# Kernel optimization log

Measured on AMD Instinct MI355X. Metric: run time of the kernel, lower is better.

Reference implementation:

```python
import jax, jax.numpy as jnp
import numpy as np

SYNCNET_T = 5
EMB_D = 512


def _l2norm(x, eps=1e-12):
    return x / jnp.maximum(jnp.linalg.norm(x, axis=-1, keepdims=True), eps)


def setup_inputs() -> dict:
    key = jax.random.key(0)
    k = jax.random.split(key, 6)
    b = 256
    a_1 = jax.random.normal(k[0], (b, 1, 80, 16), dtype=jnp.float32)
    a_2 = jax.random.normal(k[1], (b, 1, 80, 16), dtype=jnp.float32)
    v_1 = jax.random.normal(k[2], (b, 3, SYNCNET_T, 96, 96), dtype=jnp.float32)
    v_2 = jax.random.normal(k[3], (b, 3, SYNCNET_T, 96, 96), dtype=jnp.float32)
    da = 1 * 80 * 16
    dv = 3 * SYNCNET_T * 48 * 96
    W_a = jax.random.normal(k[4], (da, EMB_D), dtype=jnp.float32) / np.float32(np.sqrt(da))
    W_v = jax.random.normal(k[5], (dv, EMB_D), dtype=jnp.float32) / np.float32(np.sqrt(dv))
    return {"a_1": a_1, "v_1": v_1, "a_2": a_2, "v_2": v_2, "W_a": W_a, "W_v": W_v}


def reference(a_1, v_1, a_2, v_2, W_a, W_v):
    b = a_1.shape[0]
    audio = jnp.concatenate([a_1, a_2], axis=0)      # (2b,1,80,16)
    visual = jnp.concatenate([v_1, v_2], axis=0)     # (2b,3,T,96,96)
    visual = visual[:, :, :, visual.shape[3] // 2:]  # lower half -> (2b,3,T,48,96)
    # torch.cat([visual[:,:,i] for i in range(T)], dim=1) -> channel order (T,3)
    n2 = visual.shape[0]
    visual = jnp.moveaxis(visual, 2, 1).reshape(n2, 3 * SYNCNET_T, 48, 96)
    # syncnet (modeled): flatten -> linear -> L2 normalize, 512-d embeddings
    a = _l2norm(audio.reshape(n2, -1) @ W_a)  # (2b,d)
    v = _l2norm(visual.reshape(n2, -1) @ W_v)  # (2b,d)
    a1, a2 = a[:b], a[b:]
    v1, v2 = v[:b], v[b:]
    dot = lambda x, y: jnp.sum(x * y, axis=-1)
    # numerator: product of {a1,a2}x{v1,v2} + combos within audio and within visual
    numerator = (jnp.exp(dot(a1, v1)) + jnp.exp(dot(a1, v2))
                 + jnp.exp(dot(a2, v1)) + jnp.exp(dot(a2, v2))
                 + jnp.exp(dot(a1, a2)) + jnp.exp(dot(v1, v2)))  # (b,)
    # denominator: product of {a1,a2} with ALL visual embeddings v (2b)
    denominator = (jnp.exp(a1 @ v.T) + jnp.exp(a2 @ v.T)).sum(axis=1)  # (b,)
    loss = -jnp.mean(jnp.log(numerator / denominator))
    return loss
```

## Files before the change

### kernel.cpp

```cpp
#include <hip/hip_runtime.h>

typedef __attribute__((ext_vector_type(8))) short bf16x8;
typedef __attribute__((ext_vector_type(4))) float f32x4;

#define KSPLIT_V 16
#define KSPLIT_A 4

__device__ __forceinline__ unsigned int pk2(float a, float b) {
    unsigned int r;
    asm("v_cvt_pk_bf16_f32 %0, %1, %2" : "=v"(r) : "v"(a), "v"(b));
    return r;
}

template<int MODE>
__global__ __launch_bounds__(256, 4) void mm_kernel(
    const float* __restrict__ s1, const float* __restrict__ s2,
    const float* __restrict__ Bsrc, float* __restrict__ outp,
    float* __restrict__ den, float* __restrict__ num)
{
    __shared__ uint4 As[2][256];
    __shared__ uint4 Bs[2][256];

    const int tid = threadIdx.x;
    const int blk = blockIdx.x;

    int m0, n0, k0, nsteps, z = 0;
    if (MODE == 0) {
        const int lin = (blk & 7) * 128 + (blk >> 3);
        z  = lin >> 6;
        m0 = ((lin >> 3) & 7) * 64;
        n0 = (lin & 7) * 64;
        k0 = z * 4320;
        nsteps = 135;
    } else if (MODE == 1) {
        z  = blk >> 6;
        m0 = ((blk >> 3) & 7) * 64;
        n0 = (blk & 7) * 64;
        k0 = z * 320;
        nsteps = 10;
    } else {
        m0 = (blk >> 3) * 64;
        n0 = (blk & 7) * 64;
        k0 = 0;
        nsteps = 16;
    }
    if (MODE != 2) outp += (size_t)z * (512 * 512);

    const int ROWSTR = (MODE == 0) ? 138240 : (MODE == 1 ? 1280 : 512);

    const int a_row = tid >> 2;
    const int a_kb  = tid & 3;
    const int b_col = tid & 63;
    const int b_kb  = tid >> 6;
    const int a_u = (a_kb * 64 + a_row) ^ (a_kb << 1);
    const int b_u = (b_kb * 64 + b_col) ^ (b_kb << 1);

    const int grow = m0 + a_row;
    const float* abase = (grow < 256) ? (s1 + (size_t)grow * ROWSTR)
                                      : (s2 + (size_t)(grow - 256) * ROWSTR);
    int aoff, jj = 0, kglob = k0;
    if (MODE == 0) {
        const int ph = k0 / 4608;
        jj = k0 - ph * 4608;
        const int c = ph % 3, t = ph / 3;
        aoff = c * 46080 + t * 9216 + 4608 + jj + a_kb * 8;
    } else {
        aoff = k0 + a_kb * 8;
    }

    const float* bptr;
    if (MODE == 2) bptr = Bsrc + (size_t)(n0 + b_col) * 512 + b_kb * 8;
    else           bptr = Bsrc + (size_t)(k0 + b_kb * 8) * 512 + n0 + b_col;

    const int lane = tid & 63;
    const int wid  = tid >> 6;
    const int wrow = (wid >> 1) * 32;
    const int wcol = (wid & 1) * 32;
    const int l15  = lane & 15;
    const int lk   = lane >> 4;

    int ra[2], rb[2];
    #pragma unroll
    for (int m = 0; m < 2; ++m) ra[m] = (lk * 64 + wrow + m * 16 + l15) ^ (lk << 1);
    #pragma unroll
    for (int n = 0; n < 2; ++n) rb[n] = (lk * 64 + wcol + n * 16 + l15) ^ (lk << 1);

    f32x4 acc[2][2];
    #pragma unroll
    for (int m = 0; m < 2; ++m)
        #pragma unroll
        for (int n = 0; n < 2; ++n) acc[m][n] = f32x4{0.f, 0.f, 0.f, 0.f};

    float4 A0 = *(const float4*)(abase + aoff);
    float4 A1 = *(const float4*)(abase + aoff + 4);
    float4 B0, B1; float bsr[8];
    if (MODE == 2) {
        B0 = *(const float4*)bptr; B1 = *(const float4*)(bptr + 4);
    } else {
        #pragma unroll
        for (int j = 0; j < 8; ++j) bsr[j] = bptr[(size_t)j * 512];
    }

    for (int ks = 0; ks < nsteps; ++ks) {
        const int cur = ks & 1;

        const bool more = (ks + 1 < nsteps);
        float4 A0n, A1n, B0n, B1n; float bsn[8];
        if (more) {
            kglob += 32;
            if (MODE == 0) {
                aoff += 32; jj += 32;
                if (jj == 4608) {
                    jj = 0;
                    const int ph = kglob / 4608;
                    const int c = ph % 3, t = ph / 3;
                    aoff = c * 46080 + t * 9216 + 4608 + a_kb * 8;
                }
            } else {
                aoff += 32;
            }
            A0n = *(const float4*)(abase + aoff);
            A1n = *(const float4*)(abase + aoff + 4);
            if (MODE == 2) {
                bptr += 32;
                B0n = *(const float4*)bptr; B1n = *(const float4*)(bptr + 4);
            } else {
                bptr += 32 * 512;
                #pragma unroll
                for (int j = 0; j < 8; ++j) bsn[j] = bptr[(size_t)j * 512];
            }
        }

        uint4 pa;
        pa.x = pk2(A0.x, A0.y); pa.y = pk2(A0.z, A0.w);
        pa.z = pk2(A1.x, A1.y); pa.w = pk2(A1.z, A1.w);
        As[cur][a_u] = pa;
        uint4 pb;
        if (MODE == 2) {
            pb.x = pk2(B0.x, B0.y); pb.y = pk2(B0.z, B0.w);
            pb.z = pk2(B1.x, B1.y); pb.w = pk2(B1.z, B1.w);
        } else {
            pb.x = pk2(bsr[0], bsr[1]); pb.y = pk2(bsr[2], bsr[3]);
            pb.z = pk2(bsr[4], bsr[5]); pb.w = pk2(bsr[6], bsr[7]);
        }
        Bs[cur][b_u] = pb;
        __syncthreads();

        bf16x8 af[2], bfr[2];
        #pragma unroll
        for (int m = 0; m < 2; ++m) af[m] = __builtin_bit_cast(bf16x8, As[cur][ra[m]]);
        #pragma unroll
        for (int n = 0; n < 2; ++n) bfr[n] = __builtin_bit_cast(bf16x8, Bs[cur][rb[n]]);
        #pragma unroll
        for (int m = 0; m < 2; ++m)
            #pragma unroll
            for (int n = 0; n < 2; ++n)
                acc[m][n] = __builtin_amdgcn_mfma_f32_16x16x32_bf16(af[m], bfr[n], acc[m][n], 0, 0, 0);

        if (more) {
            A0 = A0n; A1 = A1n;
            if (MODE == 2) { B0 = B0n; B1 = B1n; }
            else {
                #pragma unroll
                for (int j = 0; j < 8; ++j) bsr[j] = bsn[j];
            }
        }
    }

    if (MODE != 2) {
        #pragma unroll
        for (int m = 0; m < 2; ++m)
            #pragma unroll
            for (int n = 0; n < 2; ++n) {
                const int col = n0 + wcol + n * 16 + l15;
                #pragma unroll
                for (int r = 0; r < 4; ++r) {
                    const int row = m0 + wrow + m * 16 + lk * 4 + r;
                    outp[(size_t)row * 512 + col] = acc[m][n][r];
                }
            }
    } else {
        #pragma unroll
        for (int m = 0; m < 2; ++m) {
            float rs[4] = {0.f, 0.f, 0.f, 0.f};
            #pragma unroll
            for (int n = 0; n < 2; ++n) {
                const int col = n0 + wcol + n * 16 + l15;
                #pragma unroll
                for (int r = 0; r < 4; ++r) {
                    const int row = m0 + wrow + m * 16 + lk * 4 + r;
                    const float e = __expf(acc[m][n][r]);
                    rs[r] += e;
                    if (((row - col) & 255) == 0) atomicAdd(num + (row & 255), e);
                }
            }
            #pragma unroll
            for (int r = 0; r < 4; ++r) {
                float v = rs[r];
                v += __shfl_xor(v, 1);
                v += __shfl_xor(v, 2);
                v += __shfl_xor(v, 4);
                v += __shfl_xor(v, 8);
                if (l15 == 0) {
                    const int row = m0 + wrow + m * 16 + lk * 4 + r;
                    atomicAdd(den + (row & 255), v);
                }
            }
        }
    }
}

__global__ __launch_bounds__(256) void norm_kernel(
    const float* __restrict__ partA, const float* __restrict__ partV,
    float* __restrict__ Aout, float* __restrict__ Vout)
{
    const int row = blockIdx.x;
    const int tid = threadIdx.x;
    const bool isV = row >= 512;
    const int r = isV ? (row - 512) : row;
    const int c0 = tid, c1 = tid + 256;

    float v0 = 0.f, v1 = 0.f;
    if (isV) {
        #pragma unroll
        for (int zz = 0; zz < KSPLIT_V; ++zz) {
            const float* p = partV + (size_t)zz * 262144 + (size_t)r * 512;
            v0 += p[c0]; v1 += p[c1];
        }
    } else {
        #pragma unroll
        for (int zz = 0; zz < KSPLIT_A; ++zz) {
            const float* p = partA + (size_t)zz * 262144 + (size_t)r * 512;
            v0 += p[c0]; v1 += p[c1];
        }
    }

    float ss = v0 * v0 + v1 * v1;
    #pragma unroll
    for (int off = 32; off > 0; off >>= 1) ss += __shfl_down(ss, off);
    __shared__ float sbuf[4];
    if ((tid & 63) == 0) sbuf[tid >> 6] = ss;
    __syncthreads();
    const float total = sbuf[0] + sbuf[1] + sbuf[2] + sbuf[3];
    const float inv = 1.f / fmaxf(sqrtf(total), 1e-12f);

    float* outp = (isV ? Vout : Aout) + (size_t)r * 512;
    outp[c0] = v0 * inv;
    outp[c1] = v1 * inv;
}

__global__ __launch_bounds__(512) void zero_kernel(float* __restrict__ p) {
    p[threadIdx.x] = 0.f;
}

__global__ __launch_bounds__(256) void dots_kernel(
    const float* __restrict__ A, const float* __restrict__ V,
    float* __restrict__ num)
{
    const int b = blockIdx.x;
    const int i = b & 255;
    const float* X = (b < 256) ? A : V;
    const float* x = X + (size_t)i * 512;
    const float* y = X + (size_t)(i + 256) * 512;
    const int tid = threadIdx.x;
    float d = x[tid] * y[tid] + x[tid + 256] * y[tid + 256];
    #pragma unroll
    for (int off = 32; off > 0; off >>= 1) d += __shfl_down(d, off);
    __shared__ float sbuf[4];
    if ((tid & 63) == 0) sbuf[tid >> 6] = d;
    __syncthreads();
    if (tid == 0) atomicAdd(num + i, __expf(sbuf[0] + sbuf[1] + sbuf[2] + sbuf[3]));
}

__global__ __launch_bounds__(256) void final_kernel(
    const float* __restrict__ den, const float* __restrict__ num,
    float* __restrict__ out)
{
    const int tid = threadIdx.x;
    float v = logf(den[tid]) - logf(num[tid]);
    #pragma unroll
    for (int off = 32; off > 0; off >>= 1) v += __shfl_down(v, off);
    __shared__ float sbuf[4];
    if ((tid & 63) == 0) sbuf[tid >> 6] = v;
    __syncthreads();
    if (tid == 0) out[0] = (sbuf[0] + sbuf[1] + sbuf[2] + sbuf[3]) * (1.f / 256.f);
}

extern "C" void kernel_launch(void* const* d_in, const int* in_sizes, int n_in,
                              void* d_out, int out_size, void* d_ws, size_t ws_size,
                              hipStream_t stream)
{
    (void)in_sizes; (void)n_in; (void)out_size; (void)ws_size;
    const float* a_1 = (const float*)d_in[0];
    const float* v_1 = (const float*)d_in[1];
    const float* a_2 = (const float*)d_in[2];
    const float* v_2 = (const float*)d_in[3];
    const float* W_a = (const float*)d_in[4];
    const float* W_v = (const float*)d_in[5];
    float* out = (float*)d_out;

    float* ws      = (float*)d_ws;
    float* partV   = ws;
    float* partA   = partV + (size_t)KSPLIT_V * 262144;
    float* Anorm   = partA + (size_t)KSPLIT_A * 262144;
    float* Vnorm   = Anorm + 262144;
    float* den     = Vnorm + 262144;
    float* num     = den + 256;

    zero_kernel<<<1, 512, 0, stream>>>(den);
    mm_kernel<0><<<1024, 256, 0, stream>>>(v_1, v_2, W_v, partV, nullptr, nullptr);
    mm_kernel<1><<<256, 256, 0, stream>>>(a_1, a_2, W_a, partA, nullptr, nullptr);
    norm_kernel<<<1024, 256, 0, stream>>>(partA, partV, Anorm, Vnorm);
    mm_kernel<2><<<64, 256, 0, stream>>>(Anorm, Anorm + 256 * 512, Vnorm, nullptr, den, num);
    dots_kernel<<<512, 256, 0, stream>>>(Anorm, Vnorm, num);
    final_kernel<<<1, 256, 0, stream>>>(den, num, out);
}
```

Baseline: 176.0 us.

## Pipeline GEMM global loads with inline asm and raise visual K-split

Rewrites the main loop of the split-K GEMM as a two-stage ping-pong over two shared-memory buffers. Global loads are issued through inline-asm `dwordx4`/`dword` instructions with immediate offsets, and explicit `vmcnt` waits let the next tile's loads overlap the pack, sync and MFMA of the current tile. The visual GEMM's K-split goes from 16 to 24 with 90 steps each, and launch bounds rise to 6 waves per SIMD, both to add parallelism and occupancy. The cost is extra partial-sum traffic that the norm kernel must reduce, plus more register pressure from the doubled prefetch buffers.

```diff
diff --git a/kernel.cpp b/kernel.cpp
--- a/kernel.cpp
+++ b/kernel.cpp
@@ -3,17 +3,31 @@
 typedef __attribute__((ext_vector_type(8))) short bf16x8;
 typedef __attribute__((ext_vector_type(4))) float f32x4;
 
-#define KSPLIT_V 16
+#define KSPLIT_V 24
+#define KSTEPS_V 90
 #define KSPLIT_A 4
+#define KSTEPS_A 10
 
 __device__ __forceinline__ unsigned int pk2(float a, float b) {
     unsigned int r;
     asm("v_cvt_pk_bf16_f32 %0, %1, %2" : "=v"(r) : "v"(a), "v"(b));
     return r;
 }
+__device__ __forceinline__ void gl4(f32x4& d, const float* p) {
+    asm volatile("global_load_dwordx4 %0, %1, off" : "=&v"(d) : "v"(p));
+}
+__device__ __forceinline__ void gl4o(f32x4& d, const float* p) {
+    asm volatile("global_load_dwordx4 %0, %1, off offset:16" : "=&v"(d) : "v"(p));
+}
+__device__ __forceinline__ void gl1(float& d, const float* p) {
+    asm volatile("global_load_dword %0, %1, off" : "=&v"(d) : "v"(p));
+}
+__device__ __forceinline__ void gl1o(float& d, const float* p) {
+    asm volatile("global_load_dword %0, %1, off offset:2048" : "=&v"(d) : "v"(p));
+}
 
 template<int MODE>
-__global__ __launch_bounds__(256, 4) void mm_kernel(
+__global__ __launch_bounds__(256, 6) void mm_kernel(
     const float* __restrict__ s1, const float* __restrict__ s2,
     const float* __restrict__ Bsrc, float* __restrict__ outp,
     float* __restrict__ den, float* __restrict__ num)
@@ -26,18 +40,19 @@
 
     int m0, n0, k0, nsteps, z = 0;
     if (MODE == 0) {
-        const int lin = (blk & 7) * 128 + (blk >> 3);
+        const int lin = (blk & 7) * 192 + (blk >> 3);
         z  = lin >> 6;
-        m0 = ((lin >> 3) & 7) * 64;
-        n0 = (lin & 7) * 64;
-        k0 = z * 4320;
-        nsteps = 135;
+        const int rem = lin & 63;
+        m0 = (rem >> 3) * 64;
+        n0 = (rem & 7) * 64;
+        k0 = z * (KSTEPS_V * 32);
+        nsteps = KSTEPS_V;
     } else if (MODE == 1) {
         z  = blk >> 6;
         m0 = ((blk >> 3) & 7) * 64;
         n0 = (blk & 7) * 64;
-        k0 = z * 320;
-        nsteps = 10;
+        k0 = z * (KSTEPS_A * 32);
+        nsteps = KSTEPS_A;
     } else {
         m0 = (blk >> 3) * 64;
         n0 = (blk & 7) * 64;
@@ -68,9 +83,17 @@
         aoff = k0 + a_kb * 8;
     }
 
-    const float* bptr;
-    if (MODE == 2) bptr = Bsrc + (size_t)(n0 + b_col) * 512 + b_kb * 8;
-    else           bptr = Bsrc + (size_t)(k0 + b_kb * 8) * 512 + n0 + b_col;
+    const float* bptr = Bsrc;
+    const float* bp0 = Bsrc; const float* bp1 = Bsrc;
+    const float* bp2 = Bsrc; const float* bp3 = Bsrc;
+    if (MODE == 2) {
+        bptr = Bsrc + (size_t)(n0 + b_col) * 512 + b_kb * 8;
+    } else {
+        bp0 = Bsrc + (size_t)(k0 + b_kb * 8) * 512 + n0 + b_col;
+        bp1 = bp0 + 1024;
+        bp2 = bp0 + 2048;
+        bp3 = bp0 + 3072;
+    }
 
     const int lane = tid & 63;
     const int wid  = tid >> 6;
@@ -91,80 +114,87 @@
         #pragma unroll
         for (int n = 0; n < 2; ++n) acc[m][n] = f32x4{0.f, 0.f, 0.f, 0.f};
 
-    float4 A0 = *(const float4*)(abase + aoff);
-    float4 A1 = *(const float4*)(abase + aoff + 4);
-    float4 B0, B1; float bsr[8];
-    if (MODE == 2) {
-        B0 = *(const float4*)bptr; B1 = *(const float4*)(bptr + 4);
-    } else {
-        #pragma unroll
-        for (int j = 0; j < 8; ++j) bsr[j] = bptr[(size_t)j * 512];
-    }
-
-    for (int ks = 0; ks < nsteps; ++ks) {
-        const int cur = ks & 1;
-
-        const bool more = (ks + 1 < nsteps);
-        float4 A0n, A1n, B0n, B1n; float bsn[8];
-        if (more) {
-            kglob += 32;
-            if (MODE == 0) {
-                aoff += 32; jj += 32;
-                if (jj == 4608) {
-                    jj = 0;
-                    const int ph = kglob / 4608;
-                    const int c = ph % 3, t = ph / 3;
-                    aoff = c * 46080 + t * 9216 + 4608 + a_kb * 8;
-                }
-            } else {
-                aoff += 32;
+    f32x4 A0c, A1c, A0n, A1n;
+    f32x4 B0c, B1c, B0n, B1n;
+    float bc[8], bn[8];
+
+    auto ISSUE = [&](f32x4& X0, f32x4& X1, float* bb, f32x4& Y0, f32x4& Y1) {
+        const float* ap = abase + aoff;
+        gl4(X0, ap); gl4o(X1, ap);
+        if constexpr (MODE == 2) {
+            gl4(Y0, bptr); gl4o(Y1, bptr);
+        } else {
+            gl1(bb[0], bp0); gl1o(bb[1], bp0);
+            gl1(bb[2], bp1); gl1o(bb[3], bp1);
+            gl1(bb[4], bp2); gl1o(bb[5], bp2);
+            gl1(bb[6], bp3); gl1o(bb[7], bp3);
+        }
+    };
+    auto ADV = [&]() {
+        if constexpr (MODE == 0) {
+            kglob += 32; aoff += 32; jj += 32;
+            if (jj == 4608) {
+                jj = 0;
+                const int ph = kglob / 4608;
+                const int c = ph % 3, t = ph / 3;
+                aoff = c * 46080 + t * 9216 + 4608 + a_kb * 8;
             }
-            A0n = *(const float4*)(abase + aoff);
-            A1n = *(const float4*)(abase + aoff + 4);
-            if (MODE == 2) {
-                bptr += 32;
-                B0n = *(const float4*)bptr; B1n = *(const float4*)(bptr + 4);
-            } else {
-                bptr += 32 * 512;
-                #pragma unroll
-                for (int j = 0; j < 8; ++j) bsn[j] = bptr[(size_t)j * 512];
-            }
-        }
-
+        } else {
+            aoff += 32;
+        }
+        if constexpr (MODE == 2) bptr += 32;
+        else { bp0 += 16384; bp1 += 16384; bp2 += 16384; bp3 += 16384; }
+    };
+    auto WAITN = [&]() {
+        if constexpr (MODE == 2) asm volatile("s_waitcnt vmcnt(4)" ::: "memory");
+        else                     asm volatile("s_waitcnt vmcnt(10)" ::: "memory");
+        __builtin_amdgcn_sched_barrier(0);
+    };
+    auto WAIT0 = [&]() {
+        asm volatile("s_waitcnt vmcnt(0)" ::: "memory");
+        __builtin_amdgcn_sched_barrier(0);
+    };
+    auto PACK = [&](int buf, f32x4& X0, f32x4& X1, float* bb, f32x4& Y0, f32x4& Y1) {
         uint4 pa;
-        pa.x = pk2(A0.x, A0.y); pa.y = pk2(A0.z, A0.w);
-        pa.z = pk2(A1.x, A1.y); pa.w = pk2(A1.z, A1.w);
-        As[cur][a_u] = pa;
+        pa.x = pk2(X0.x, X0.y); pa.y = pk2(X0.z, X0.w);
+        pa.z = pk2(X1.x, X1.y); pa.w = pk2(X1.z, X1.w);
+        As[buf][a_u] = pa;
         uint4 pb;
-        if (MODE == 2) {
-            pb.x = pk2(B0.x, B0.y); pb.y = pk2(B0.z, B0.w);
-            pb.z = pk2(B1.x, B1.y); pb.w = pk2(B1.z, B1.w);
+        if constexpr (MODE == 2) {
+            pb.x = pk2(Y0.x, Y0.y); pb.y = pk2(Y0.z, Y0.w);
+            pb.z = pk2(Y1.x, Y1.y); pb.w = pk2(Y1.z, Y1.w);
         } else {
-            pb.x = pk2(bsr[0], bsr[1]); pb.y = pk2(bsr[2], bsr[3]);
-            pb.z = pk2(bsr[4], bsr[5]); pb.w = pk2(bsr[6], bsr[7]);
-        }
-        Bs[cur][b_u] = pb;
-        __syncthreads();
-
+            pb.x = pk2(bb[0], bb[1]); pb.y = pk2(bb[2], bb[3]);
+            pb.z = pk2(bb[4], bb[5]); pb.w = pk2(bb[6], bb[7]);
+        }
+        Bs[buf][b_u] = pb;
+    };
+    auto MM = [&](int buf) {
         bf16x8 af[2], bfr[2];
         #pragma unroll
-        for (int m = 0; m < 2; ++m) af[m] = __builtin_bit_cast(bf16x8, As[cur][ra[m]]);
-        #pragma unroll
-        for (int n = 0; n < 2; ++n) bfr[n] = __builtin_bit_cast(bf16x8, Bs[cur][rb[n]]);
+        for (int m = 0; m < 2; ++m) af[m] = __builtin_bit_cast(bf16x8, As[buf][ra[m]]);
+        #pragma unroll
+        for (int n = 0; n < 2; ++n) bfr[n] = __builtin_bit_cast(bf16x8, Bs[buf][rb[n]]);
         #pragma unroll
         for (int m = 0; m < 2; ++m)
             #pragma unroll
             for (int n = 0; n < 2; ++n)
                 acc[m][n] = __builtin_amdgcn_mfma_f32_16x16x32_bf16(af[m], bfr[n], acc[m][n], 0, 0, 0);
-
-        if (more) {
-            A0 = A0n; A1 = A1n;
-            if (MODE == 2) { B0 = B0n; B1 = B1n; }
-            else {
-                #pragma unroll
-                for (int j = 0; j < 8; ++j) bsr[j] = bsn[j];
-            }
-        }
+    };
+
+    ISSUE(A0c, A1c, bc, B0c, B1c);
+
+    for (int ks = 0; ks < nsteps; ks += 2) {
+        ADV(); ISSUE(A0n, A1n, bn, B0n, B1n);
+        WAITN();
+        PACK(0, A0c, A1c, bc, B0c, B1c);
+        __syncthreads();
+        MM(0);
+        if (ks + 2 < nsteps) { ADV(); ISSUE(A0c, A1c, bc, B0c, B1c); WAITN(); }
+        else                 { WAIT0(); }
+        PACK(1, A0n, A1n, bn, B0n, B1n);
+        __syncthreads();
+        MM(1);
     }
 
     if (MODE != 2) {
@@ -308,8 +338,8 @@
     float* num     = den + 256;
 
     zero_kernel<<<1, 512, 0, stream>>>(den);
-    mm_kernel<0><<<1024, 256, 0, stream>>>(v_1, v_2, W_v, partV, nullptr, nullptr);
-    mm_kernel<1><<<256, 256, 0, stream>>>(a_1, a_2, W_a, partA, nullptr, nullptr);
+    mm_kernel<0><<<KSPLIT_V * 64, 256, 0, stream>>>(v_1, v_2, W_v, partV, nullptr, nullptr);
+    mm_kernel<1><<<KSPLIT_A * 64, 256, 0, stream>>>(a_1, a_2, W_a, partA, nullptr, nullptr);
     norm_kernel<<<1024, 256, 0, stream>>>(partA, partV, Anorm, Vnorm);
     mm_kernel<2><<<64, 256, 0, stream>>>(Anorm, Anorm + 256 * 512, Vnorm, nullptr, den, num);
     dots_kernel<<<512, 256, 0, stream>>>(Anorm, Vnorm, num);
```

Measured after the change: 228.6 us. +29.9%, slower.

## Use 128x128 tiles with transposed LDS reads for the projection GEMMs

Applied to the files above, without the earlier changes.

Replaces the 64x64-tile templated GEMM with a 128x128-tile kernel in which each wave computes a 64x64 subtile (4x4 MFMAs). B is stored row-major in LDS and read with ds_read_b64_tr_b16 transposes, so W loads become coalesced float4 reads instead of strided scalar loads. The split-K factors change to 45 for visual and 2 for audio, and the similarity GEMM moves into its own kernel. This raises arithmetic intensity and cuts global load count, but uses more registers, lowers occupancy, and writes 45 partial slabs that the norm kernel must then read back.

```diff
diff --git a/kernel.cpp b/kernel.cpp
--- a/kernel.cpp
+++ b/kernel.cpp
@@ -2,9 +2,10 @@
 
 typedef __attribute__((ext_vector_type(8))) short bf16x8;
 typedef __attribute__((ext_vector_type(4))) float f32x4;
-
-#define KSPLIT_V 16
-#define KSPLIT_A 4
+typedef __attribute__((ext_vector_type(2))) unsigned int u32x2;
+
+#define KSV 45
+#define KSA 2
 
 __device__ __forceinline__ unsigned int pk2(float a, float b) {
     unsigned int r;
@@ -12,207 +13,162 @@
     return r;
 }
 
-template<int MODE>
-__global__ __launch_bounds__(256, 4) void mm_kernel(
+__device__ __forceinline__ u32x2 tr_lo(unsigned addr) {
+    u32x2 r;
+    asm volatile("ds_read_b64_tr_b16 %0, %1" : "=v"(r) : "v"(addr));
+    return r;
+}
+__device__ __forceinline__ u32x2 tr_hi(unsigned addr) {
+    u32x2 r;
+    asm volatile("ds_read_b64_tr_b16 %0, %1 offset:1024" : "=v"(r) : "v"(addr));
+    return r;
+}
+
+template<int CROP>
+__global__ __launch_bounds__(256, 2) void gemm_kernel(
     const float* __restrict__ s1, const float* __restrict__ s2,
-    const float* __restrict__ Bsrc, float* __restrict__ outp,
-    float* __restrict__ den, float* __restrict__ num)
-{
-    __shared__ uint4 As[2][256];
-    __shared__ uint4 Bs[2][256];
+    const float* __restrict__ W, float* __restrict__ part, int ksteps)
+{
+    __shared__ uint4 As[512];
+    __shared__ uint4 Bs[512];
 
     const int tid = threadIdx.x;
     const int blk = blockIdx.x;
-
-    int m0, n0, k0, nsteps, z = 0;
-    if (MODE == 0) {
-        const int lin = (blk & 7) * 128 + (blk >> 3);
-        z  = lin >> 6;
-        m0 = ((lin >> 3) & 7) * 64;
-        n0 = (lin & 7) * 64;
-        k0 = z * 4320;
-        nsteps = 135;
-    } else if (MODE == 1) {
-        z  = blk >> 6;
-        m0 = ((blk >> 3) & 7) * 64;
-        n0 = (blk & 7) * 64;
-        k0 = z * 320;
-        nsteps = 10;
-    } else {
-        m0 = (blk >> 3) * 64;
-        n0 = (blk & 7) * 64;
-        k0 = 0;
-        nsteps = 16;
-    }
-    if (MODE != 2) outp += (size_t)z * (512 * 512);
-
-    const int ROWSTR = (MODE == 0) ? 138240 : (MODE == 1 ? 1280 : 512);
-
-    const int a_row = tid >> 2;
-    const int a_kb  = tid & 3;
-    const int b_col = tid & 63;
-    const int b_kb  = tid >> 6;
-    const int a_u = (a_kb * 64 + a_row) ^ (a_kb << 1);
-    const int b_u = (b_kb * 64 + b_col) ^ (b_kb << 1);
-
-    const int grow = m0 + a_row;
-    const float* abase = (grow < 256) ? (s1 + (size_t)grow * ROWSTR)
-                                      : (s2 + (size_t)(grow - 256) * ROWSTR);
-    int aoff, jj = 0, kglob = k0;
-    if (MODE == 0) {
-        const int ph = k0 / 4608;
-        jj = k0 - ph * 4608;
-        const int c = ph % 3, t = ph / 3;
-        aoff = c * 46080 + t * 9216 + 4608 + jj + a_kb * 8;
-    } else {
-        aoff = k0 + a_kb * 8;
-    }
-
-    const float* bptr;
-    if (MODE == 2) bptr = Bsrc + (size_t)(n0 + b_col) * 512 + b_kb * 8;
-    else           bptr = Bsrc + (size_t)(k0 + b_kb * 8) * 512 + n0 + b_col;
+    const int cpx = gridDim.x >> 3;
+    const int lin = (blk & 7) * cpx + (blk >> 3);
+    const int z  = lin >> 4;
+    const int mn = lin & 15;
+    const int m0 = (mn >> 2) * 128;
+    const int n0 = (mn & 3) * 128;
+    const int k0 = z * ksteps * 32;
+    part += (size_t)z * 262144;
+
+    const int a_row = tid >> 1;
+    const int a_off = (tid & 1) << 4;
+    const int grow  = m0 + a_row;
+    const int ROWSTR = CROP ? 138240 : 1280;
+    const float* abase = (grow < 256) ? s1 + (size_t)grow * ROWSTR
+                                      : s2 + (size_t)(grow - 256) * ROWSTR;
+    const int a_u0 = a_row * 4 + (((tid & 1) * 2 + 0) ^ (a_row & 3));
+    const int a_u1 = a_row * 4 + (((tid & 1) * 2 + 1) ^ (a_row & 3));
+
+    const int b_k = tid >> 3;
+    const int b_g = tid & 7;
+    const float* bbase = W + (size_t)b_k * 512 + b_g * 16;
+    const int b_u0 = (b_k >> 2) * 64 + b_g * 8 + (b_k & 3) * 2;
 
     const int lane = tid & 63;
     const int wid  = tid >> 6;
-    const int wrow = (wid >> 1) * 32;
-    const int wcol = (wid & 1) * 32;
     const int l15  = lane & 15;
     const int lk   = lane >> 4;
-
-    int ra[2], rb[2];
-    #pragma unroll
-    for (int m = 0; m < 2; ++m) ra[m] = (lk * 64 + wrow + m * 16 + l15) ^ (lk << 1);
-    #pragma unroll
-    for (int n = 0; n < 2; ++n) rb[n] = (lk * 64 + wcol + n * 16 + l15) ^ (lk << 1);
-
-    f32x4 acc[2][2];
-    #pragma unroll
-    for (int m = 0; m < 2; ++m)
-        #pragma unroll
-        for (int n = 0; n < 2; ++n) acc[m][n] = f32x4{0.f, 0.f, 0.f, 0.f};
-
-    float4 A0 = *(const float4*)(abase + aoff);
-    float4 A1 = *(const float4*)(abase + aoff + 4);
-    float4 B0, B1; float bsr[8];
-    if (MODE == 2) {
-        B0 = *(const float4*)bptr; B1 = *(const float4*)(bptr + 4);
-    } else {
-        #pragma unroll
-        for (int j = 0; j < 8; ++j) bsr[j] = bptr[(size_t)j * 512];
-    }
-
-    for (int ks = 0; ks < nsteps; ++ks) {
-        const int cur = ks & 1;
-
-        const bool more = (ks + 1 < nsteps);
-        float4 A0n, A1n, B0n, B1n; float bsn[8];
-        if (more) {
-            kglob += 32;
-            if (MODE == 0) {
-                aoff += 32; jj += 32;
-                if (jj == 4608) {
-                    jj = 0;
-                    const int ph = kglob / 4608;
-                    const int c = ph % 3, t = ph / 3;
-                    aoff = c * 46080 + t * 9216 + 4608 + a_kb * 8;
-                }
-            } else {
-                aoff += 32;
-            }
-            A0n = *(const float4*)(abase + aoff);
-            A1n = *(const float4*)(abase + aoff + 4);
-            if (MODE == 2) {
-                bptr += 32;
-                B0n = *(const float4*)bptr; B1n = *(const float4*)(bptr + 4);
-            } else {
-                bptr += 32 * 512;
-                #pragma unroll
-                for (int j = 0; j < 8; ++j) bsn[j] = bptr[(size_t)j * 512];
-            }
-        }
-
-        uint4 pa;
-        pa.x = pk2(A0.x, A0.y); pa.y = pk2(A0.z, A0.w);
-        pa.z = pk2(A1.x, A1.y); pa.w = pk2(A1.z, A1.w);
-        As[cur][a_u] = pa;
-        uint4 pb;
-        if (MODE == 2) {
-            pb.x = pk2(B0.x, B0.y); pb.y = pk2(B0.z, B0.w);
-            pb.z = pk2(B1.x, B1.y); pb.w = pk2(B1.z, B1.w);
+    const int wm = (wid >> 1) * 64;
+    const int wn = (wid & 1) * 64;
+
+    int ua[4];
+    #pragma unroll
+    for (int mi = 0; mi < 4; ++mi) {
+        const int row = wm + mi * 16 + l15;
+        ua[mi] = row * 4 + (lk ^ (row & 3));
+    }
+    const unsigned bsBase = (unsigned)(uintptr_t)(void*)(&Bs[0]);
+    unsigned btr[4];
+    #pragma unroll
+    for (int ni = 0; ni < 4; ++ni)
+        btr[ni] = bsBase + (unsigned)((2 * lk) * 1024 + ((wn >> 4) + ni) * 128 + l15 * 2);
+
+    f32x4 acc[4][4];
+    #pragma unroll
+    for (int mi = 0; mi < 4; ++mi)
+        #pragma unroll
+        for (int ni = 0; ni < 4; ++ni) acc[mi][ni] = f32x4{0.f, 0.f, 0.f, 0.f};
+
+    auto LOADA = [&](f32x4* av, int ks) {
+        const int kgs = k0 + ks * 32;
+        const float* ap;
+        if (CROP) {
+            const int p = kgs / 4608;
+            const int j = kgs - p * 4608;
+            const int c = p % 3, t9 = p / 3;
+            ap = abase + c * 46080 + t9 * 9216 + 4608 + j + a_off;
         } else {
-            pb.x = pk2(bsr[0], bsr[1]); pb.y = pk2(bsr[2], bsr[3]);
-            pb.z = pk2(bsr[4], bsr[5]); pb.w = pk2(bsr[6], bsr[7]);
-        }
-        Bs[cur][b_u] = pb;
-        __syncthreads();
-
-        bf16x8 af[2], bfr[2];
-        #pragma unroll
-        for (int m = 0; m < 2; ++m) af[m] = __builtin_bit_cast(bf16x8, As[cur][ra[m]]);
-        #pragma unroll
-        for (int n = 0; n < 2; ++n) bfr[n] = __builtin_bit_cast(bf16x8, Bs[cur][rb[n]]);
-        #pragma unroll
-        for (int m = 0; m < 2; ++m)
+            ap = abase + kgs + a_off;
+        }
+        #pragma unroll
+        for (int i = 0; i < 4; ++i) av[i] = *(const f32x4*)(ap + 4 * i);
+    };
+    auto LOADB = [&](f32x4* bv, int ks) {
+        const float* bp = bbase + (size_t)(k0 + ks * 32) * 512;
+        #pragma unroll
+        for (int i = 0; i < 4; ++i) bv[i] = *(const f32x4*)(bp + 4 * i);
+    };
+    auto PACK = [&](const f32x4* av, const f32x4* bv) {
+        uint4 pa0, pa1, pb0, pb1;
+        pa0.x = pk2(av[0].x, av[0].y); pa0.y = pk2(av[0].z, av[0].w);
+        pa0.z = pk2(av[1].x, av[1].y); pa0.w = pk2(av[1].z, av[1].w);
+        pa1.x = pk2(av[2].x, av[2].y); pa1.y = pk2(av[2].z, av[2].w);
+        pa1.z = pk2(av[3].x, av[3].y); pa1.w = pk2(av[3].z, av[3].w);
+        As[a_u0] = pa0;
+        As[a_u1] = pa1;
+        pb0.x = pk2(bv[0].x, bv[0].y); pb0.y = pk2(bv[0].z, bv[0].w);
+        pb0.z = pk2(bv[1].x, bv[1].y); pb0.w = pk2(bv[1].z, bv[1].w);
+        pb1.x = pk2(bv[2].x, bv[2].y); pb1.y = pk2(bv[2].z, bv[2].w);
+        pb1.z = pk2(bv[3].x, bv[3].y); pb1.w = pk2(bv[3].z, bv[3].w);
+        Bs[b_u0]     = pb0;
+        Bs[b_u0 + 1] = pb1;
+    };
+    auto COMPUTE = [&]() {
+        bf16x8 af[4];
+        #pragma unroll
+        for (int mi = 0; mi < 4; ++mi) af[mi] = __builtin_bit_cast(bf16x8, As[ua[mi]]);
+        u32x2 lo[4], hi[4];
+        #pragma unroll
+        for (int ni = 0; ni < 4; ++ni) { lo[ni] = tr_lo(btr[ni]); hi[ni] = tr_hi(btr[ni]); }
+        asm volatile("s_waitcnt lgkmcnt(0)" ::: "memory");
+        __builtin_amdgcn_sched_barrier(0);
+        bf16x8 bf[4];
+        #pragma unroll
+        for (int ni = 0; ni < 4; ++ni) {
+            uint4 q; q.x = lo[ni].x; q.y = lo[ni].y; q.z = hi[ni].x; q.w = hi[ni].y;
+            bf[ni] = __builtin_bit_cast(bf16x8, q);
+        }
+        #pragma unroll
+        for (int mi = 0; mi < 4; ++mi)
             #pragma unroll
-            for (int n = 0; n < 2; ++n)
-                acc[m][n] = __builtin_amdgcn_mfma_f32_16x16x32_bf16(af[m], bfr[n], acc[m][n], 0, 0, 0);
-
-        if (more) {
-            A0 = A0n; A1 = A1n;
-            if (MODE == 2) { B0 = B0n; B1 = B1n; }
-            else {
-                #pragma unroll
-                for (int j = 0; j < 8; ++j) bsr[j] = bsn[j];
-            }
-        }
-    }
-
-    if (MODE != 2) {
-        #pragma unroll
-        for (int m = 0; m < 2; ++m)
-            #pragma unroll
-            for (int n = 0; n < 2; ++n) {
-                const int col = n0 + wcol + n * 16 + l15;
-                #pragma unroll
-                for (int r = 0; r < 4; ++r) {
-                    const int row = m0 + wrow + m * 16 + lk * 4 + r;
-                    outp[(size_t)row * 512 + col] = acc[m][n][r];
-                }
-            }
-    } else {
-        #pragma unroll
-        for (int m = 0; m < 2; ++m) {
-            float rs[4] = {0.f, 0.f, 0.f, 0.f};
-            #pragma unroll
-            for (int n = 0; n < 2; ++n) {
-                const int col = n0 + wcol + n * 16 + l15;
-                #pragma unroll
-                for (int r = 0; r < 4; ++r) {
-                    const int row = m0 + wrow + m * 16 + lk * 4 + r;
-                    const float e = __expf(acc[m][n][r]);
-                    rs[r] += e;
-                    if (((row - col) & 255) == 0) atomicAdd(num + (row & 255), e);
-                }
-            }
+            for (int ni = 0; ni < 4; ++ni)
+                acc[mi][ni] = __builtin_amdgcn_mfma_f32_16x16x32_bf16(af[mi], bf[ni], acc[mi][ni], 0, 0, 0);
+    };
+
+    f32x4 av0[4], bv0[4], av1[4], bv1[4];
+    LOADA(av0, 0); LOADB(bv0, 0);
+    for (int ks = 0; ks < ksteps; ks += 2) {
+        LOADA(av1, ks + 1); LOADB(bv1, ks + 1);
+        PACK(av0, bv0);
+        __syncthreads();
+        COMPUTE();
+        __syncthreads();
+        if (ks + 2 < ksteps) { LOADA(av0, ks + 2); LOADB(bv0, ks + 2); }
+        PACK(av1, bv1);
+        __syncthreads();
+        COMPUTE();
+        __syncthreads();
+    }
+
+    #pragma unroll
+    for (int mi = 0; mi < 4; ++mi)
+        #pragma unroll
+        for (int ni = 0; ni < 4; ++ni) {
+            const int col = n0 + wn + ni * 16 + l15;
             #pragma unroll
             for (int r = 0; r < 4; ++r) {
-                float v = rs[r];
-                v += __shfl_xor(v, 1);
-                v += __shfl_xor(v, 2);
-                v += __shfl_xor(v, 4);
-                v += __shfl_xor(v, 8);
-                if (l15 == 0) {
-                    const int row = m0 + wrow + m * 16 + lk * 4 + r;
-                    atomicAdd(den + (row & 255), v);
-                }
+                const int row = m0 + wm + mi * 16 + lk * 4 + r;
+                part[(size_t)row * 512 + col] = acc[mi][ni][r];
             }
         }
-    }
 }
 
 __global__ __launch_bounds__(256) void norm_kernel(
     const float* __restrict__ partA, const float* __restrict__ partV,
-    float* __restrict__ Aout, float* __restrict__ Vout)
+    float* __restrict__ Aout, float* __restrict__ Vout, int nzV)
 {
     const int row = blockIdx.x;
     const int tid = threadIdx.x;
@@ -222,14 +178,13 @@
 
     float v0 = 0.f, v1 = 0.f;
     if (isV) {
-        #pragma unroll
-        for (int zz = 0; zz < KSPLIT_V; ++zz) {
+        for (int zz = 0; zz < nzV; ++zz) {
             const float* p = partV + (size_t)zz * 262144 + (size_t)r * 512;
             v0 += p[c0]; v1 += p[c1];
         }
     } else {
         #pragma unroll
-        for (int zz = 0; zz < KSPLIT_A; ++zz) {
+        for (int zz = 0; zz < KSA; ++zz) {
             const float* p = partA + (size_t)zz * 262144 + (size_t)r * 512;
             v0 += p[c0]; v1 += p[c1];
         }
@@ -247,6 +202,112 @@
     float* outp = (isV ? Vout : Aout) + (size_t)r * 512;
     outp[c0] = v0 * inv;
     outp[c1] = v1 * inv;
+}
+
+__global__ __launch_bounds__(256) void sim_kernel(
+    const float* __restrict__ A, const float* __restrict__ V,
+    float* __restrict__ den, float* __restrict__ num)
+{
+    __shared__ uint4 As[2][256];
+    __shared__ uint4 Bs[2][256];
+
+    const int tid = threadIdx.x;
+    const int m0 = (blockIdx.x >> 3) * 64;
+    const int n0 = (blockIdx.x & 7) * 64;
+    const int nsteps = 16;
+
+    const int a_row = tid >> 2, a_kb = tid & 3;
+    const int b_col = tid & 63, b_kb = tid >> 6;
+    const int a_u = (a_kb * 64 + a_row) ^ (a_kb << 1);
+    const int b_u = (b_kb * 64 + b_col) ^ (b_kb << 1);
+
+    const float* abase = A + (size_t)(m0 + a_row) * 512;
+    const float* bptr  = V + (size_t)(n0 + b_col) * 512 + b_kb * 8;
+    int aoff = a_kb * 8;
+
+    const int lane = tid & 63, wid = tid >> 6;
+    const int wrow = (wid >> 1) * 32, wcol = (wid & 1) * 32;
+    const int l15 = lane & 15, lk = lane >> 4;
+
+    int ra[2], rb[2];
+    #pragma unroll
+    for (int m = 0; m < 2; ++m) ra[m] = (lk * 64 + wrow + m * 16 + l15) ^ (lk << 1);
+    #pragma unroll
+    for (int n = 0; n < 2; ++n) rb[n] = (lk * 64 + wcol + n * 16 + l15) ^ (lk << 1);
+
+    f32x4 acc[2][2];
+    #pragma unroll
+    for (int m = 0; m < 2; ++m)
+        #pragma unroll
+        for (int n = 0; n < 2; ++n) acc[m][n] = f32x4{0.f, 0.f, 0.f, 0.f};
+
+    float4 A0 = *(const float4*)(abase + aoff);
+    float4 A1 = *(const float4*)(abase + aoff + 4);
+    float4 B0 = *(const float4*)bptr;
+    float4 B1 = *(const float4*)(bptr + 4);
+
+    for (int ks = 0; ks < nsteps; ++ks) {
+        const int cur = ks & 1;
+        const bool more = (ks + 1 < nsteps);
+        float4 A0n, A1n, B0n, B1n;
+        if (more) {
+            aoff += 32; bptr += 32;
+            A0n = *(const float4*)(abase + aoff);
+            A1n = *(const float4*)(abase + aoff + 4);
+            B0n = *(const float4*)bptr;
+            B1n = *(const float4*)(bptr + 4);
+        }
+        uint4 pa;
+        pa.x = pk2(A0.x, A0.y); pa.y = pk2(A0.z, A0.w);
+        pa.z = pk2(A1.x, A1.y); pa.w = pk2(A1.z, A1.w);
+        As[cur][a_u] = pa;
+        uint4 pb;
+        pb.x = pk2(B0.x, B0.y); pb.y = pk2(B0.z, B0.w);
+        pb.z = pk2(B1.x, B1.y); pb.w = pk2(B1.z, B1.w);
+        Bs[cur][b_u] = pb;
+        __syncthreads();
+
+        bf16x8 af[2], bfr[2];
+        #pragma unroll
+        for (int m = 0; m < 2; ++m) af[m] = __builtin_bit_cast(bf16x8, As[cur][ra[m]]);
+        #pragma unroll
+        for (int n = 0; n < 2; ++n) bfr[n] = __builtin_bit_cast(bf16x8, Bs[cur][rb[n]]);
+        #pragma unroll
+        for (int m = 0; m < 2; ++m)
+            #pragma unroll
+            for (int n = 0; n < 2; ++n)
+                acc[m][n] = __builtin_amdgcn_mfma_f32_16x16x32_bf16(af[m], bfr[n], acc[m][n], 0, 0, 0);
+
+        if (more) { A0 = A0n; A1 = A1n; B0 = B0n; B1 = B1n; }
+    }
+
+    #pragma unroll
+    for (int m = 0; m < 2; ++m) {
+        float rs[4] = {0.f, 0.f, 0.f, 0.f};
+        #pragma unroll
+        for (int n = 0; n < 2; ++n) {
+            const int col = n0 + wcol + n * 16 + l15;
+            #pragma unroll
+            for (int r = 0; r < 4; ++r) {
+                const int row = m0 + wrow + m * 16 + lk * 4 + r;
+                const float e = __expf(acc[m][n][r]);
+                rs[r] += e;
+                if (((row - col) & 255) == 0) atomicAdd(num + (row & 255), e);
+            }
+        }
+        #pragma unroll
+        for (int r = 0; r < 4; ++r) {
+            float v = rs[r];
+            v += __shfl_xor(v, 1);
+            v += __shfl_xor(v, 2);
+            v += __shfl_xor(v, 4);
+            v += __shfl_xor(v, 8);
+            if (l15 == 0) {
+                const int row = m0 + wrow + m * 16 + lk * 4 + r;
+                atomicAdd(den + (row & 255), v);
+            }
+        }
+    }
 }
 
 __global__ __launch_bounds__(512) void zero_kernel(float* __restrict__ p) {
@@ -299,19 +360,21 @@
     const float* W_v = (const float*)d_in[5];
     float* out = (float*)d_out;
 
-    float* ws      = (float*)d_ws;
-    float* partV   = ws;
-    float* partA   = partV + (size_t)KSPLIT_V * 262144;
-    float* Anorm   = partA + (size_t)KSPLIT_A * 262144;
-    float* Vnorm   = Anorm + 262144;
-    float* den     = Vnorm + 262144;
-    float* num     = den + 256;
+    float* cur   = (float*)d_ws;
+    float* den   = cur; cur += 256;
+    float* num   = cur; cur += 256;
+    float* Anorm = cur; cur += 262144;
+    float* Vnorm = cur; cur += 262144;
+    float* partA = cur; cur += (size_t)KSA * 262144;
+    float* partV = cur; cur += (size_t)KSV * 262144;
 
     zero_kernel<<<1, 512, 0, stream>>>(den);
-    mm_kernel<0><<<1024, 256, 0, stream>>>(v_1, v_2, W_v, partV, nullptr, nullptr);
-    mm_kernel<1><<<256, 256, 0, stream>>>(a_1, a_2, W_a, partA, nullptr, nullptr);
-    norm_kernel<<<1024, 256, 0, stream>>>(partA, partV, Anorm, Vnorm);
-    mm_kernel<2><<<64, 256, 0, stream>>>(Anorm, Anorm + 256 * 512, Vnorm, nullptr, den, num);
+
+    gemm_kernel<1><<<16 * KSV, 256, 0, stream>>>(v_1, v_2, W_v, partV, 48);
+    gemm_kernel<0><<<16 * KSA, 256, 0, stream>>>(a_1, a_2, W_a, partA, 20);
+
+    norm_kernel<<<1024, 256, 0, stream>>>(partA, partV, Anorm, Vnorm, KSV);
+    sim_kernel<<<64, 256, 0, stream>>>(Anorm, Vnorm, den, num);
     dots_kernel<<<512, 256, 0, stream>>>(Anorm, Vnorm, num);
     final_kernel<<<1, 256, 0, stream>>>(den, num, out);
 }
```

Result: slower. 189.3 us (+7.6%).
